# Optimization experiments

Hardware: AMD Instinct MI355X
Metric: run time of the kernel (lower is better)

The kernel has to match this reference:

```python
import jax, jax.numpy as jnp
import numpy as np

B, C, H, W = 8, 256, 128, 128
KC, VC, HEADS = 256, 256, 8


def setup_inputs() -> dict:
    key = jax.random.key(0)
    ks = jax.random.split(key, 10)
    s = 0.05
    return {
        "x": jax.random.normal(ks[0], (B, C, H, W), jnp.float32),
        "Wk": jax.random.normal(ks[1], (KC, C), jnp.float32) * s,
        "bk": jax.random.normal(ks[2], (KC,), jnp.float32) * s,
        "Wq": jax.random.normal(ks[3], (KC, C), jnp.float32) * s,
        "bq": jax.random.normal(ks[4], (KC,), jnp.float32) * s,
        "Wv": jax.random.normal(ks[5], (VC, C), jnp.float32) * s,
        "bv": jax.random.normal(ks[6], (VC,), jnp.float32) * s,
        "Wr": jax.random.normal(ks[7], (C, VC), jnp.float32) * s,
        "br": jax.random.normal(ks[8], (C,), jnp.float32) * s,
        "head_count": HEADS,
    }


def reference(x, Wk, bk, Wq, bq, Wv, bv, Wr, br, head_count):
    n, c, h, w = x.shape
    hw = h * w
    xf = x.reshape(n, c, hw)  # [n, C, S]
    # 1x1 convs == per-pixel linear projections
    keys = jnp.einsum('kc,ncs->nks', Wk, xf) + bk[None, :, None]
    queries = jnp.einsum('kc,ncs->nks', Wq, xf) + bq[None, :, None]
    values = jnp.einsum('vc,ncs->nvs', Wv, xf) + bv[None, :, None]

    dk = Wk.shape[0] // head_count
    dv = Wv.shape[0] // head_count
    # split heads along channel dim (matches torch channel slicing)
    K = jax.nn.softmax(keys.reshape(n, head_count, dk, hw), axis=-1)   # softmax over spatial
    Q = jax.nn.softmax(queries.reshape(n, head_count, dk, hw), axis=2) # softmax over key dim
    V = values.reshape(n, head_count, dv, hw)

    # context = K @ V^T : [n, h, dk, dv]
    ctx = jnp.einsum('nhks,nhvs->nhkv', K, V)
    # attended = ctx^T @ Q : [n, h, dv, S]
    att = jnp.einsum('nhkv,nhks->nhvs', ctx, Q).reshape(n, head_count * dv, h, w)

    attention = jnp.einsum('ov,nvhw->nohw', Wr, att) + br[None, :, None, None]
    # attention map: per-head mean over key dim, then mean over heads
    attention_map = K.mean(axis=2).mean(axis=1).reshape(n, h, w)
    # torch returns the LAST head's context (loop variable after the loop)
    context_last = ctx[:, -1]
    return attention, context_last, attention_map
```

## Files before the change

### kernel.cpp

```cpp
#include <hip/hip_runtime.h>
#include <hip/hip_bf16.h>

typedef float f32x4 __attribute__((ext_vector_type(4)));
typedef short s16x8 __attribute__((ext_vector_type(8)));
typedef short s16x4 __attribute__((ext_vector_type(4)));
typedef __bf16 bf16x8 __attribute__((ext_vector_type(8)));
typedef unsigned short u16;

#define DEVI __device__ __forceinline__

static constexpr int    HW      = 16384;
static constexpr size_t BSTRIDE = (size_t)256 * HW;

static constexpr size_t oXBT   = 0;
static constexpr size_t oEK    = oXBT  + (size_t)8 * HW * 256 * 2;
static constexpr size_t oQT    = oEK   + (size_t)8 * 256 * HW * 2;
static constexpr size_t oVB    = oQT   + (size_t)8 * HW * 256 * 2;
static constexpr size_t oWK    = oVB   + (size_t)8 * 256 * HW * 2;
static constexpr size_t oBIAS  = oWK   + (size_t)768 * 256 * 2;
static constexpr size_t oISE   = oBIAS + 4096;
static constexpr size_t oPS    = oISE  + 8192;
static constexpr size_t oCTX   = oPS   + (size_t)256 * 2048 * 4;
static constexpr size_t oMB    = oCTX  + (size_t)64 * 1024 * 4;
static constexpr size_t oCPART = oMB   + (size_t)8 * 256 * 256 * 2;
static constexpr size_t oMPART = oCPART + (size_t)4096 * 1024 * 4;

DEVI float bf2f(short x) {
  unsigned u = ((unsigned)(unsigned short)x) << 16;
  return __builtin_bit_cast(float, u);
}
DEVI u16 f2bf(float x) { return __builtin_bit_cast(u16, (__bf16)x); }

DEVI void gld16(const void* g, void* l) {
  __builtin_amdgcn_global_load_lds(
      (__attribute__((address_space(1))) void*)(g),
      (__attribute__((address_space(3))) void*)(l), 16, 0, 0);
}

__global__ __launch_bounds__(256) void k_prep(
    const float* __restrict__ Wk, const float* __restrict__ Wq, const float* __restrict__ Wv,
    const float* __restrict__ bk, const float* __restrict__ bq, const float* __restrict__ bv,
    u16* __restrict__ Wkqv, float* __restrict__ bias)
{
  int i = blockIdx.x * 256 + threadIdx.x;
  for (int p = i; p < 768 * 256; p += 64 * 256) {
    float v = (p < 65536) ? Wk[p] : (p < 131072 ? Wq[p - 65536] : Wv[p - 131072]);
    Wkqv[p] = f2bf(v);
  }
  if (i < 768) bias[i] = (i < 256) ? bk[i] : (i < 512 ? bq[i - 256] : bv[i - 512]);
}

__global__ __launch_bounds__(256) void k_transpose(const float* __restrict__ in_, u16* __restrict__ out)
{
  __shared__ u16 lds[64 * 256];
  const int t = threadIdx.x;
  const int n = blockIdx.y;
  const int s0 = blockIdx.x * 64;
  const float* src = in_ + ((size_t)n * 256 + t) * HW + s0;
  #pragma unroll
  for (int i = 0; i < 16; ++i) {
    f32x4 v = *(const f32x4*)(src + i * 4);
    #pragma unroll
    for (int j = 0; j < 4; ++j) lds[(i * 4 + j) * 256 + t] = f2bf(v[j]);
  }
  __syncthreads();
  s16x8* gp = (s16x8*)(out + (size_t)n * BSTRIDE + (size_t)s0 * 256);
  const s16x8* lp = (const s16x8*)lds;
  #pragma unroll
  for (int i = 0; i < 8; ++i) gp[t + i * 256] = lp[t + i * 256];
}


__global__ __launch_bounds__(256, 2) void k_projKV(
    const u16* __restrict__ W, const u16* __restrict__ xbT, const float* __restrict__ bias,
    u16* __restrict__ ek, u16* __restrict__ vb, float* __restrict__ ps)
{
  __shared__ u16 smem[32768];
  const int t = threadIdx.x;
  const int L = blockIdx.x;
  const int n = L & 7;
  const int idx = L >> 3;
  const int mbi = idx & 3;
  const int sq  = idx >> 2;
  const bool isK = (mbi < 2);
  const int m0 = (mbi & 1) * 128;
  const int aBase = (isK ? 0 : 512) + m0;
  const int lane = t & 63;
  const int l15 = lane & 15, l4 = (lane >> 4) & 3;
  const int wv = t >> 6;
  const int wm = (wv & 1) * 64, wn = (wv >> 1) * 64;
  const u16* Ab = W + (size_t)aBase * 256;
  const u16* Bb = xbT + (size_t)n * BSTRIDE;
  u16* Al = smem;
  u16* Bl = smem + 16384;

  float biasv[4];
  #pragma unroll
  for (int mf = 0; mf < 4; ++mf) biasv[mf] = bias[aBase + wm + mf * 16 + l15];

  const int rr = t >> 3;
  const int csh = t & 7;
  auto STAGE = [&](int buf, int it) {
    const int k0 = (it & 3) * 64;
    const size_t s_t0 = (size_t)((sq * 4 + (it >> 2)) * 128);
    #pragma unroll
    for (int i = 0; i < 4; ++i) {
      const int row = i * 32 + rr;
      const int cs = (csh ^ (row & 7)) * 8;
      gld16(Ab + (size_t)row * 256 + k0 + cs,          Al + buf * 8192 + i * 2048 + t * 8);
      gld16(Bb + (s_t0 + row) * 256 + k0 + cs,         Bl + buf * 8192 + i * 2048 + t * 8);
    }
  };

  f32x4 acc[4][4] = {};
  STAGE(0, 0); STAGE(1, 1);

  u16* outb = (isK ? ek : vb) + (size_t)n * BSTRIDE;

  #pragma unroll
  for (int it = 0; it < 16; ++it) {
    if (it == 15)                          asm volatile("s_waitcnt vmcnt(0)" ::: "memory");
    else if ((it & 3) <= 1 && it >= 4) {
      if (isK) asm volatile("s_waitcnt vmcnt(28)" ::: "memory");
      else     asm volatile("s_waitcnt vmcnt(24)" ::: "memory");
    } else                                 asm volatile("s_waitcnt vmcnt(8)" ::: "memory");
    __builtin_amdgcn_s_barrier();

    const int buf = it & 1;
    #pragma unroll
    for (int ks = 0; ks < 2; ++ks) {
      bf16x8 af[4], bff[4];
      #pragma unroll
      for (int g = 0; g < 4; ++g) {
        const int mrow = wm + g * 16 + l15;
        const int srow = wn + g * 16 + l15;
        af[g]  = *(const bf16x8*)&Al[buf * 8192 + mrow * 64 + (((ks * 4 + l4) ^ (mrow & 7)) * 8)];
        bff[g] = *(const bf16x8*)&Bl[buf * 8192 + srow * 64 + (((ks * 4 + l4) ^ (srow & 7)) * 8)];
      }
      __builtin_amdgcn_s_setprio(1);
      #pragma unroll
      for (int sf = 0; sf < 4; ++sf)
        #pragma unroll
        for (int mf = 0; mf < 4; ++mf)
          acc[sf][mf] = __builtin_amdgcn_mfma_f32_16x16x32_bf16(bff[sf], af[mf], acc[sf][mf], 0, 0, 0);
      __builtin_amdgcn_s_setprio(0);
    }
    asm volatile("s_waitcnt lgkmcnt(0)" ::: "memory");
    __builtin_amdgcn_s_barrier();
    if (it < 14) STAGE(buf, it + 2);

    if ((it & 3) == 3) {
      const int tile = it >> 2;
      const int s0t = (sq * 4 + tile) * 128;
      const int stile = sq * 4 + tile;
      if (isK) {
        float rs[4] = {0.f, 0.f, 0.f, 0.f};
        #pragma unroll
        for (int sf = 0; sf < 4; ++sf)
          #pragma unroll
          for (int mf = 0; mf < 4; ++mf) {
            s16x4 pk;
            #pragma unroll
            for (int r = 0; r < 4; ++r) {
              const float e = __expf(acc[sf][mf][r] + biasv[mf]);
              rs[mf] += e;
              pk[r] = (short)f2bf(e);
            }
            *(s16x4*)(outb + (size_t)(m0 + wm + mf * 16 + l15) * HW + s0t + wn + sf * 16 + l4 * 4) = pk;
          }
        #pragma unroll
        for (int mf = 0; mf < 4; ++mf) {
          float v = rs[mf];
          v += __shfl_xor(v, 16); v += __shfl_xor(v, 32);
          if (l4 == 0)
            ps[((size_t)(stile * 2 + (wn >> 6))) * 2048 + n * 256 + m0 + wm + mf * 16 + l15] = v;
        }
      } else {
        #pragma unroll
        for (int sf = 0; sf < 4; ++sf)
          #pragma unroll
          for (int mf = 0; mf < 4; ++mf) {
            s16x4 pk;
            #pragma unroll
            for (int r = 0; r < 4; ++r) pk[r] = (short)f2bf(acc[sf][mf][r] + biasv[mf]);
            *(s16x4*)(outb + (size_t)(m0 + wm + mf * 16 + l15) * HW + s0t + wn + sf * 16 + l4 * 4) = pk;
          }
      }
      #pragma unroll
      for (int sf = 0; sf < 4; ++sf)
        #pragma unroll
        for (int mf = 0; mf < 4; ++mf) acc[sf][mf] = f32x4{0.f, 0.f, 0.f, 0.f};
    }
  }
}

__global__ __launch_bounds__(256, 2) void k_attn2(
    const u16* __restrict__ Mb, const u16* __restrict__ qT, const float* __restrict__ br,
    float* __restrict__ Out)
{
  __shared__ u16 smem[32768];
  const int t = threadIdx.x;
  const int L = blockIdx.x;
  const int n = L & 7;
  const int idx = L >> 3;
  const int mb = idx & 1;
  const int sq = idx >> 1;
  const int m0 = mb * 128;
  const int lane = t & 63;
  const int l15 = lane & 15, l4 = (lane >> 4) & 3;
  const int wv = t >> 6;
  const int wm = (wv & 1) * 64, wn = (wv >> 1) * 64;
  const u16* Ab = Mb + (size_t)n * 65536 + (size_t)m0 * 256;
  const u16* Bb = qT + (size_t)n * BSTRIDE;
  u16* Al = smem;
  u16* Bl = smem + 16384;

  float biasv[4];
  #pragma unroll
  for (int mf = 0; mf < 4; ++mf) biasv[mf] = br[m0 + wm + mf * 16 + l15];

  const int rr = t >> 3;
  const int csh = t & 7;
  auto STAGE = [&](int buf, int it) {
    const int k0 = (it & 3) * 64;
    const size_t s_t0 = (size_t)((sq * 4 + (it >> 2)) * 128);
    #pragma unroll
    for (int i = 0; i < 4; ++i) {
      const int row = i * 32 + rr;
      const int cs = (csh ^ (row & 7)) * 8;
      gld16(Ab + (size_t)row * 256 + k0 + cs,  Al + buf * 8192 + i * 2048 + t * 8);
      gld16(Bb + (s_t0 + row) * 256 + k0 + cs, Bl + buf * 8192 + i * 2048 + t * 8);
    }
  };

  f32x4 acc[4][4] = {};
  STAGE(0, 0); STAGE(1, 1);

  float* ob = Out + (size_t)n * BSTRIDE;

  #pragma unroll
  for (int it = 0; it < 16; ++it) {
    if (it == 15)                          asm volatile("s_waitcnt vmcnt(0)" ::: "memory");
    else if ((it & 3) <= 1 && it >= 4)     asm volatile("s_waitcnt vmcnt(24)" ::: "memory");
    else                                   asm volatile("s_waitcnt vmcnt(8)" ::: "memory");
    __builtin_amdgcn_s_barrier();

    const int buf = it & 1;
    #pragma unroll
    for (int ks = 0; ks < 2; ++ks) {
      bf16x8 af[4], bff[4];
      #pragma unroll
      for (int g = 0; g < 4; ++g) {
        const int mrow = wm + g * 16 + l15;
        const int srow = wn + g * 16 + l15;
        af[g]  = *(const bf16x8*)&Al[buf * 8192 + mrow * 64 + (((ks * 4 + l4) ^ (mrow & 7)) * 8)];
        bff[g] = *(const bf16x8*)&Bl[buf * 8192 + srow * 64 + (((ks * 4 + l4) ^ (srow & 7)) * 8)];
      }
      __builtin_amdgcn_s_setprio(1);
      #pragma unroll
      for (int sf = 0; sf < 4; ++sf)
        #pragma unroll
        for (int mf = 0; mf < 4; ++mf)
          acc[sf][mf] = __builtin_amdgcn_mfma_f32_16x16x32_bf16(bff[sf], af[mf], acc[sf][mf], 0, 0, 0);
      __builtin_amdgcn_s_setprio(0);
    }
    asm volatile("s_waitcnt lgkmcnt(0)" ::: "memory");
    __builtin_amdgcn_s_barrier();
    if (it < 14) STAGE(buf, it + 2);

    if ((it & 3) == 3) {
      const int s0t = (sq * 4 + (it >> 2)) * 128;
      #pragma unroll
      for (int sf = 0; sf < 4; ++sf)
        #pragma unroll
        for (int mf = 0; mf < 4; ++mf) {
          f32x4 o = acc[sf][mf] + biasv[mf];
          *(f32x4*)(ob + (size_t)(m0 + wm + mf * 16 + l15) * HW + s0t + wn + sf * 16 + l4 * 4) = o;
          acc[sf][mf] = f32x4{0.f, 0.f, 0.f, 0.f};
        }
    }
  }
}

#define GEMM_CORE(Ab, Bb)                                                                   \
  u16* Al = smem;                                                                           \
  u16* Bl = smem + 16384;                                                                   \
  auto STAGE = [&](int buf, int kt) {                                                       \
    const int k0 = kt * 64;                                                                 \
    _Pragma("unroll")                                                                       \
    for (int i = 0; i < 4; ++i) {                                                           \
      const int r_ = i * 32 + (t >> 3);                                                     \
      const int cs = (((t & 7) ^ (r_ & 7)) * 8);                                            \
      gld16((Ab) + (size_t)r_ * 256 + k0 + cs, Al + buf * 8192 + i * 2048 + t * 8);         \
      gld16((Bb) + (size_t)r_ * 256 + k0 + cs, Bl + buf * 8192 + i * 2048 + t * 8);         \
    }                                                                                       \
  };                                                                                        \
  f32x4 acc[4][4] = {};                                                                     \
  STAGE(0, 0); STAGE(1, 1);                                                                 \
  _Pragma("unroll")                                                                         \
  for (int kt = 0; kt < 4; ++kt) {                                                          \
    if (kt < 3) asm volatile("s_waitcnt vmcnt(8)" ::: "memory");                            \
    else        asm volatile("s_waitcnt vmcnt(0)" ::: "memory");                            \
    __builtin_amdgcn_s_barrier();                                                           \
    const int buf = kt & 1;                                                                 \
    _Pragma("unroll")                                                                       \
    for (int ks = 0; ks < 2; ++ks) {                                                        \
      bf16x8 af[4], bff[4];                                                                 \
      _Pragma("unroll")                                                                     \
      for (int g = 0; g < 4; ++g) {                                                         \
        const int mrow = wm + g * 16 + l15;                                                 \
        const int srow = wn + g * 16 + l15;                                                 \
        af[g]  = *(const bf16x8*)&Al[buf * 8192 + mrow * 64 + (((ks * 4 + l4) ^ (mrow & 7)) * 8)]; \
        bff[g] = *(const bf16x8*)&Bl[buf * 8192 + srow * 64 + (((ks * 4 + l4) ^ (srow & 7)) * 8)]; \
      }                                                                                     \
      __builtin_amdgcn_s_setprio(1);                                                        \
      _Pragma("unroll")                                                                     \
      for (int mg = 0; mg < 4; ++mg)                                                        \
        _Pragma("unroll")                                                                   \
        for (int ng = 0; ng < 4; ++ng)                                                      \
          acc[mg][ng] = __builtin_amdgcn_mfma_f32_16x16x32_bf16(af[mg], bff[ng], acc[mg][ng], 0, 0, 0); \
      __builtin_amdgcn_s_setprio(0);                                                        \
    }                                                                                       \
    asm volatile("s_waitcnt lgkmcnt(0)" ::: "memory");                                      \
    __builtin_amdgcn_s_barrier();                                                           \
    if (kt < 2) STAGE(buf, kt + 2);                                                         \
  }

__global__ __launch_bounds__(256, 2) void k_projQ(
    const u16* __restrict__ W, const u16* __restrict__ xbT, const float* __restrict__ bias,
    u16* __restrict__ qT)
{
  __shared__ u16 smem[32768];
  const int t = threadIdx.x;
  const int L = blockIdx.x;
  const int n  = L & 7;
  const int idx = L >> 3;
  const int mbq = idx & 1;
  const int sb  = idx >> 1;
  const int m0 = 256 + mbq * 128, s0 = sb * 128;
  const int lane = t & 63;
  const int l15 = lane & 15, l4 = (lane >> 4) & 3;
  const int wv = t >> 6;
  const int wm = (wv & 1) * 64, wn = (wv >> 1) * 64;
  const u16* Ab = W + (size_t)m0 * 256;
  const u16* Bb = xbT + (size_t)n * BSTRIDE + (size_t)s0 * 256;

  GEMM_CORE(Ab, Bb)

  #pragma unroll
  for (int mg = 0; mg < 4; ++mg)
    #pragma unroll
    for (int r = 0; r < 4; ++r) {
      const float bb = bias[m0 + wm + mg * 16 + l4 * 4 + r];
      #pragma unroll
      for (int ng = 0; ng < 4; ++ng) acc[mg][ng][r] += bb;
    }

  #pragma unroll
  for (int hh = 0; hh < 2; ++hh)
    #pragma unroll
    for (int ng = 0; ng < 4; ++ng) {
      float s = 0.f;
      #pragma unroll
      for (int mg = hh * 2; mg < hh * 2 + 2; ++mg)
        #pragma unroll
        for (int r = 0; r < 4; ++r) { const float e = __expf(acc[mg][ng][r]); acc[mg][ng][r] = e; s += e; }
      s += __shfl_xor(s, 16);
      s += __shfl_xor(s, 32);
      const float inv = 1.f / s;
      #pragma unroll
      for (int mg = hh * 2; mg < hh * 2 + 2; ++mg)
        #pragma unroll
        for (int r = 0; r < 4; ++r) acc[mg][ng][r] *= inv;
    }
  __syncthreads();
  #pragma unroll
  for (int mg = 0; mg < 4; ++mg)
    #pragma unroll
    for (int ng = 0; ng < 4; ++ng)
      #pragma unroll
      for (int r = 0; r < 4; ++r) {
        const int srow = wn + ng * 16 + l15;
        const int mcol = wm + mg * 16 + l4 * 4 + r;
        smem[srow * 136 + mcol] = f2bf(acc[mg][ng][r]);
      }
  __syncthreads();
  u16* O = qT + (size_t)n * BSTRIDE + (size_t)s0 * 256 + mbq * 128;
  #pragma unroll
  for (int it = 0; it < 8; ++it) {
    const int row = it * 16 + (t >> 4);
    *(s16x8*)(O + (size_t)row * 256 + (t & 15) * 8) = *(const s16x8*)&smem[row * 136 + (t & 15) * 8];
  }
}

__global__ __launch_bounds__(256) void k_inv(const float* __restrict__ ps, float* __restrict__ ise)
{
  const int i = blockIdx.x * 256 + threadIdx.x;
  float s = 0.f;
  for (int b = 0; b < 256; ++b) s += ps[(size_t)b * 2048 + i];
  ise[i] = 1.f / s;
}

__global__ __launch_bounds__(64) void k_ctx_part(
    const u16* __restrict__ ek, const u16* __restrict__ vb, const float* __restrict__ ise,
    float* __restrict__ cpart, float* __restrict__ mpart)
{
  const int blk = blockIdx.x;
  const int chunk = blk & 63, nh = blk >> 6;
  const int h = nh & 7, n = nh >> 3;
  const int lane = threadIdx.x;
  const int l15 = lane & 15, l4 = lane >> 4;
  const u16* kb = ek + ((size_t)n * 256 + h * 32) * HW;
  const u16* vv = vb + ((size_t)n * 256 + h * 32) * HW;
  const float iv0 = ise[n * 256 + h * 32 + l15];
  const float iv1 = ise[n * 256 + h * 32 + 16 + l15];
  f32x4 acc[2][2] = {};
  float macc[8][8] = {};
  const int sbase = chunk * 256 + l4 * 8;
  #pragma unroll
  for (int ks = 0; ks < 8; ++ks) {
    const int sb = sbase + ks * 32;
    bf16x8 ef[2], vf[2];
    #pragma unroll
    for (int g = 0; g < 2; ++g) {
      ef[g] = *(const bf16x8*)(kb + (size_t)(g * 16 + l15) * HW + sb);
      vf[g] = *(const bf16x8*)(vv + (size_t)(g * 16 + l15) * HW + sb);
    }
    #pragma unroll
    for (int j = 0; j < 8; ++j)
      macc[ks][j] = fmaf(iv0, (float)ef[0][j], fmaf(iv1, (float)ef[1][j], macc[ks][j]));
    #pragma unroll
    for (int a = 0; a < 2; ++a)
      #pragma unroll
      for (int b = 0; b < 2; ++b)
        acc[a][b] = __builtin_amdgcn_mfma_f32_16x16x32_bf16(ef[a], vf[b], acc[a][b], 0, 0, 0);
  }
  float* op = cpart + (size_t)blk * 1024;
  #pragma unroll
  for (int a = 0; a < 2; ++a)
    #pragma unroll
    for (int b = 0; b < 2; ++b)
      #pragma unroll
      for (int r = 0; r < 4; ++r)
        op[(a * 16 + l4 * 4 + r) * 32 + b * 16 + l15] = acc[a][b][r];
  #pragma unroll
  for (int ks = 0; ks < 8; ++ks)
    #pragma unroll
    for (int j = 0; j < 8; ++j) {
      float v = macc[ks][j];
      v += __shfl_xor(v, 1); v += __shfl_xor(v, 2);
      v += __shfl_xor(v, 4); v += __shfl_xor(v, 8);
      macc[ks][j] = v;
    }
  if (l15 == 0) {
    float* mp = mpart + ((size_t)h * 8 + n) * HW + sbase;
    #pragma unroll
    for (int ks = 0; ks < 8; ++ks) {
      f32x4 a = {macc[ks][0], macc[ks][1], macc[ks][2], macc[ks][3]};
      f32x4 b = {macc[ks][4], macc[ks][5], macc[ks][6], macc[ks][7]};
      *(f32x4*)(mp + ks * 32)     = a;
      *(f32x4*)(mp + ks * 32 + 4) = b;
    }
  }
}

__global__ __launch_bounds__(256) void k_ctx_reduce(
    const float* __restrict__ cpart, const float* __restrict__ ise,
    float* __restrict__ ctx, float* __restrict__ dctx)
{
  const int nh = blockIdx.x, n = nh >> 3, h = nh & 7, t = threadIdx.x;
  f32x4 a = {};
  for (int c = 0; c < 64; ++c) a += *(const f32x4*)(cpart + ((size_t)nh * 64 + c) * 1024 + t * 4);
  const float inv = ise[n * 256 + h * 32 + (t >> 3)];
  a *= inv;
  *(f32x4*)(ctx + (size_t)nh * 1024 + t * 4) = a;
  if (h == 7) *(f32x4*)(dctx + (size_t)n * 1024 + t * 4) = a;
}

__global__ __launch_bounds__(256) void k_mmat(
    const float* __restrict__ ctx, const float* __restrict__ Wr, u16* __restrict__ Mb)
{
  const int nh = blockIdx.x, n = nh >> 3, h = nh & 7, o = threadIdx.x;
  __shared__ float cl[1024];
  #pragma unroll
  for (int i = 0; i < 4; ++i) cl[o + i * 256] = ctx[(size_t)nh * 1024 + o + i * 256];
  __syncthreads();
  float wr[32];
  const float* wp = Wr + (size_t)o * 256 + h * 32;
  #pragma unroll
  for (int v = 0; v < 32; ++v) wr[v] = wp[v];
  u16* mp = Mb + ((size_t)n * 256 + o) * 256 + h * 32;
  #pragma unroll 4
  for (int k = 0; k < 32; ++k) {
    float s = 0.f;
    #pragma unroll
    for (int v = 0; v < 32; ++v) s += wr[v] * cl[k * 32 + v];
    mp[k] = f2bf(s);
  }
}

__global__ __launch_bounds__(256) void k_map_reduce(const float* __restrict__ mpart, float* __restrict__ dmap)
{
  const int i = blockIdx.x * 256 + threadIdx.x;
  f32x4 a = {};
  #pragma unroll
  for (int h = 0; h < 8; ++h) a += *(const f32x4*)(mpart + (size_t)h * 131072 + (size_t)i * 4);
  a *= (1.0f / 256.0f);
  *(f32x4*)(dmap + (size_t)i * 4) = a;
}

extern "C" void kernel_launch(void* const* d_in, const int* in_sizes, int n_in,
                              void* d_out, int out_size, void* d_ws, size_t ws_size,
                              hipStream_t stream)
{
  (void)in_sizes; (void)n_in; (void)out_size; (void)ws_size;
  const float* x  = (const float*)d_in[0];
  const float* Wk = (const float*)d_in[1];
  const float* bk = (const float*)d_in[2];
  const float* Wq = (const float*)d_in[3];
  const float* bq = (const float*)d_in[4];
  const float* Wv = (const float*)d_in[5];
  const float* bv = (const float*)d_in[6];
  const float* Wr = (const float*)d_in[7];
  const float* br = (const float*)d_in[8];

  char* ws = (char*)d_ws;
  u16*   xbT  = (u16*)(ws + oXBT);
  u16*   ek   = (u16*)(ws + oEK);
  u16*   qT   = (u16*)(ws + oQT);
  u16*   vb   = (u16*)(ws + oVB);
  u16*   Wkqv = (u16*)(ws + oWK);
  float* bias = (float*)(ws + oBIAS);
  float* ise  = (float*)(ws + oISE);
  float* ps   = (float*)(ws + oPS);
  float* ctx  = (float*)(ws + oCTX);
  u16*   Mb   = (u16*)(ws + oMB);
  float* cpart= (float*)(ws + oCPART);
  float* mpart= (float*)(ws + oMPART);

  float* attn = (float*)d_out;
  float* dctx = (float*)d_out + 33554432;
  float* dmap = (float*)d_out + 33562624;

  k_prep<<<64, 256, 0, stream>>>(Wk, Wq, Wv, bk, bq, bv, Wkqv, bias);
  k_transpose<<<dim3(256, 8), 256, 0, stream>>>(x, xbT);
  k_projKV<<<1024, 256, 0, stream>>>(Wkqv, xbT, bias, ek, vb, ps);
  k_inv<<<8, 256, 0, stream>>>(ps, ise);
  k_projQ<<<2048, 256, 0, stream>>>(Wkqv, xbT, bias, qT);
  k_ctx_part<<<4096, 64, 0, stream>>>(ek, vb, ise, cpart, mpart);
  k_ctx_reduce<<<64, 256, 0, stream>>>(cpart, ise, ctx, dctx);
  k_mmat<<<64, 256, 0, stream>>>(ctx, Wr, Mb);
  k_map_reduce<<<128, 256, 0, stream>>>(mpart, dmap);
  k_attn2<<<512, 256, 0, stream>>>(Mb, qT, br, attn);
}
```

Baseline: 289.7 us.

## Merge K/V and Q projections into one 256x256-tile 8-wave GEMM kernel

```diff
diff --git a/kernel.cpp b/kernel.cpp
--- a/kernel.cpp
+++ b/kernel.cpp
@@ -70,126 +70,175 @@
   for (int i = 0; i < 8; ++i) gp[t + i * 256] = lp[t + i * 256];
 }
 
-
-__global__ __launch_bounds__(256, 2) void k_projKV(
+__global__ __launch_bounds__(512, 2) void k_proj8(
     const u16* __restrict__ W, const u16* __restrict__ xbT, const float* __restrict__ bias,
-    u16* __restrict__ ek, u16* __restrict__ vb, float* __restrict__ ps)
-{
-  __shared__ u16 smem[32768];
+    u16* __restrict__ ek, u16* __restrict__ qT, u16* __restrict__ vb, float* __restrict__ ps)
+{
+  __shared__ u16 smem[65536];
   const int t = threadIdx.x;
   const int L = blockIdx.x;
   const int n = L & 7;
   const int idx = L >> 3;
-  const int mbi = idx & 3;
-  const int sq  = idx >> 2;
-  const bool isK = (mbi < 2);
-  const int m0 = (mbi & 1) * 128;
-  const int aBase = (isK ? 0 : 512) + m0;
+  const int mb = idx % 3;
+  const int sb = idx / 3;
   const int lane = t & 63;
   const int l15 = lane & 15, l4 = (lane >> 4) & 3;
-  const int wv = t >> 6;
-  const int wm = (wv & 1) * 64, wn = (wv >> 1) * 64;
-  const u16* Ab = W + (size_t)aBase * 256;
-  const u16* Bb = xbT + (size_t)n * BSTRIDE;
-  u16* Al = smem;
-  u16* Bl = smem + 16384;
-
-  float biasv[4];
-  #pragma unroll
-  for (int mf = 0; mf < 4; ++mf) biasv[mf] = bias[aBase + wm + mf * 16 + l15];
-
-  const int rr = t >> 3;
-  const int csh = t & 7;
-  auto STAGE = [&](int buf, int it) {
-    const int k0 = (it & 3) * 64;
-    const size_t s_t0 = (size_t)((sq * 4 + (it >> 2)) * 128);
-    #pragma unroll
-    for (int i = 0; i < 4; ++i) {
-      const int row = i * 32 + rr;
-      const int cs = (csh ^ (row & 7)) * 8;
-      gld16(Ab + (size_t)row * 256 + k0 + cs,          Al + buf * 8192 + i * 2048 + t * 8);
-      gld16(Bb + (s_t0 + row) * 256 + k0 + cs,         Bl + buf * 8192 + i * 2048 + t * 8);
+  const int w = t >> 6;
+  const int wr = w & 1, wc = w >> 1;
+
+  const u16* Ag = W + (size_t)mb * 65536;
+  const u16* Bg = xbT + (size_t)n * BSTRIDE;
+
+  float biasv[8];
+  #pragma unroll
+  for (int mf = 0; mf < 8; ++mf) biasv[mf] = bias[mb * 256 + wr * 128 + mf * 16 + l15];
+
+  const int srow8 = t >> 3, schk = t & 7;
+
+  auto STAGE = [&](int kt, int u) {
+    const int buf = kt & 1;
+    const int h = u & 1;
+    const int k0 = (kt & 3) * 64;
+    #pragma unroll
+    for (int i = 0; i < 2; ++i) {
+      const int rl = h * 128 + i * 64 + srow8;
+      const int cs = (schk ^ (rl & 7)) * 8;
+      if (u < 2) {
+        gld16(Bg + ((size_t)((sb * 2 + (kt >> 2)) * 256 + rl)) * 256 + k0 + cs,
+              smem + 32768 + buf * 16384 + h * 8192 + i * 4096 + t * 8);
+      } else {
+        gld16(Ag + (size_t)rl * 256 + k0 + cs,
+              smem + buf * 16384 + h * 8192 + i * 4096 + t * 8);
+      }
     }
   };
 
-  f32x4 acc[4][4] = {};
-  STAGE(0, 0); STAGE(1, 1);
-
-  u16* outb = (isK ? ek : vb) + (size_t)n * BSTRIDE;
-
-  #pragma unroll
-  for (int it = 0; it < 16; ++it) {
-    if (it == 15)                          asm volatile("s_waitcnt vmcnt(0)" ::: "memory");
-    else if ((it & 3) <= 1 && it >= 4) {
-      if (isK) asm volatile("s_waitcnt vmcnt(28)" ::: "memory");
-      else     asm volatile("s_waitcnt vmcnt(24)" ::: "memory");
-    } else                                 asm volatile("s_waitcnt vmcnt(8)" ::: "memory");
-    __builtin_amdgcn_s_barrier();
-
-    const int buf = it & 1;
-    #pragma unroll
-    for (int ks = 0; ks < 2; ++ks) {
-      bf16x8 af[4], bff[4];
-      #pragma unroll
-      for (int g = 0; g < 4; ++g) {
-        const int mrow = wm + g * 16 + l15;
-        const int srow = wn + g * 16 + l15;
-        af[g]  = *(const bf16x8*)&Al[buf * 8192 + mrow * 64 + (((ks * 4 + l4) ^ (mrow & 7)) * 8)];
-        bff[g] = *(const bf16x8*)&Bl[buf * 8192 + srow * 64 + (((ks * 4 + l4) ^ (srow & 7)) * 8)];
-      }
+  f32x4 acc[8][4] = {};
+  bf16x8 bff[4][2];
+
+  STAGE(0, 0); STAGE(0, 1); STAGE(0, 2); STAGE(0, 3);
+
+  u16* ekb = ek + (size_t)n * BSTRIDE;
+  u16* vbb = vb + (size_t)n * BSTRIDE;
+  u16* qtb = qT + (size_t)n * BSTRIDE;
+
+  #pragma unroll
+  for (int kt = 0; kt < 8; ++kt) {
+    const int buf = kt & 1;
+    #pragma unroll
+    for (int q = 0; q < 4; ++q) {
+      if (q == 0) {
+        if (kt < 7) STAGE(kt + 1, 0);
+        if (kt == 0)      asm volatile("s_waitcnt vmcnt(2)" ::: "memory");
+        else if (kt == 7) asm volatile("s_waitcnt vmcnt(0)" ::: "memory");
+        else if (kt == 4) {
+          if (mb == 0)      asm volatile("s_waitcnt vmcnt(42)" ::: "memory");
+          else if (mb == 2) asm volatile("s_waitcnt vmcnt(34)" ::: "memory");
+          else              asm volatile("s_waitcnt vmcnt(63)" ::: "memory");
+        }
+        else              asm volatile("s_waitcnt vmcnt(2)" ::: "memory");
+        __builtin_amdgcn_s_barrier();
+        #pragma unroll
+        for (int sf = 0; sf < 4; ++sf) {
+          const int srow = wc * 64 + sf * 16 + l15;
+          #pragma unroll
+          for (int ks = 0; ks < 2; ++ks)
+            bff[sf][ks] = *(const bf16x8*)&smem[32768 + buf * 16384 + srow * 64 +
+                                                (((ks * 4 + l4) ^ (srow & 7)) * 8)];
+        }
+      }
+      bf16x8 af[2][2];
+      #pragma unroll
+      for (int j = 0; j < 2; ++j) {
+        const int mrow = wr * 128 + (q * 2 + j) * 16 + l15;
+        #pragma unroll
+        for (int ks = 0; ks < 2; ++ks)
+          af[j][ks] = *(const bf16x8*)&smem[buf * 16384 + mrow * 64 +
+                                            (((ks * 4 + l4) ^ (mrow & 7)) * 8)];
+      }
+      if (q > 0) {
+        if (kt < 7) STAGE(kt + 1, q);
+        __builtin_amdgcn_s_barrier();
+      }
+      asm volatile("s_waitcnt lgkmcnt(0)" ::: "memory");
+      __builtin_amdgcn_sched_barrier(0);
       __builtin_amdgcn_s_setprio(1);
       #pragma unroll
-      for (int sf = 0; sf < 4; ++sf)
-        #pragma unroll
-        for (int mf = 0; mf < 4; ++mf)
-          acc[sf][mf] = __builtin_amdgcn_mfma_f32_16x16x32_bf16(bff[sf], af[mf], acc[sf][mf], 0, 0, 0);
-      __builtin_amdgcn_s_setprio(0);
-    }
-    asm volatile("s_waitcnt lgkmcnt(0)" ::: "memory");
-    __builtin_amdgcn_s_barrier();
-    if (it < 14) STAGE(buf, it + 2);
-
-    if ((it & 3) == 3) {
-      const int tile = it >> 2;
-      const int s0t = (sq * 4 + tile) * 128;
-      const int stile = sq * 4 + tile;
-      if (isK) {
-        float rs[4] = {0.f, 0.f, 0.f, 0.f};
+      for (int j = 0; j < 2; ++j)
         #pragma unroll
         for (int sf = 0; sf < 4; ++sf)
           #pragma unroll
-          for (int mf = 0; mf < 4; ++mf) {
+          for (int ks = 0; ks < 2; ++ks)
+            acc[q * 2 + j][sf] = __builtin_amdgcn_mfma_f32_16x16x32_bf16(
+                bff[sf][ks], af[j][ks], acc[q * 2 + j][sf], 0, 0, 0);
+      __builtin_amdgcn_s_setprio(0);
+      __builtin_amdgcn_s_barrier();
+    }
+
+    if ((kt & 3) == 3) {
+      const int st = kt >> 2;
+      const int s0t = (sb * 2 + st) * 256 + wc * 64;
+      const int slot = (sb * 2 + st) * 4 + wc;
+      if (mb == 0) {
+        float rs[8];
+        #pragma unroll
+        for (int mf = 0; mf < 8; ++mf) rs[mf] = 0.f;
+        #pragma unroll
+        for (int mf = 0; mf < 8; ++mf) {
+          const size_t rb = (size_t)(wr * 128 + mf * 16 + l15) * HW + s0t;
+          #pragma unroll
+          for (int sf = 0; sf < 4; ++sf) {
             s16x4 pk;
             #pragma unroll
             for (int r = 0; r < 4; ++r) {
-              const float e = __expf(acc[sf][mf][r] + biasv[mf]);
+              const float e = __expf(acc[mf][sf][r] + biasv[mf]);
               rs[mf] += e;
               pk[r] = (short)f2bf(e);
             }
-            *(s16x4*)(outb + (size_t)(m0 + wm + mf * 16 + l15) * HW + s0t + wn + sf * 16 + l4 * 4) = pk;
+            *(s16x4*)(ekb + rb + sf * 16 + l4 * 4) = pk;
           }
-        #pragma unroll
-        for (int mf = 0; mf < 4; ++mf) {
+        }
+        #pragma unroll
+        for (int mf = 0; mf < 8; ++mf) {
           float v = rs[mf];
           v += __shfl_xor(v, 16); v += __shfl_xor(v, 32);
-          if (l4 == 0)
-            ps[((size_t)(stile * 2 + (wn >> 6))) * 2048 + n * 256 + m0 + wm + mf * 16 + l15] = v;
-        }
-      } else {
-        #pragma unroll
-        for (int sf = 0; sf < 4; ++sf)
+          if (l4 == 0) ps[(size_t)slot * 2048 + n * 256 + wr * 128 + mf * 16 + l15] = v;
+        }
+      } else if (mb == 2) {
+        #pragma unroll
+        for (int mf = 0; mf < 8; ++mf) {
+          const size_t rb = (size_t)(wr * 128 + mf * 16 + l15) * HW + s0t;
           #pragma unroll
-          for (int mf = 0; mf < 4; ++mf) {
+          for (int sf = 0; sf < 4; ++sf) {
             s16x4 pk;
             #pragma unroll
-            for (int r = 0; r < 4; ++r) pk[r] = (short)f2bf(acc[sf][mf][r] + biasv[mf]);
-            *(s16x4*)(outb + (size_t)(m0 + wm + mf * 16 + l15) * HW + s0t + wn + sf * 16 + l4 * 4) = pk;
+            for (int r = 0; r < 4; ++r) pk[r] = (short)f2bf(acc[mf][sf][r] + biasv[mf]);
+            *(s16x4*)(vbb + rb + sf * 16 + l4 * 4) = pk;
           }
-      }
-      #pragma unroll
-      for (int sf = 0; sf < 4; ++sf)
-        #pragma unroll
-        for (int mf = 0; mf < 4; ++mf) acc[sf][mf] = f32x4{0.f, 0.f, 0.f, 0.f};
+        }
+      } else {
+        #pragma unroll
+        for (int hh = 0; hh < 4; ++hh) {
+          #pragma unroll
+          for (int sf = 0; sf < 4; ++sf)
+            #pragma unroll
+            for (int r = 0; r < 4; ++r) {
+              const float e0 = __expf(acc[2 * hh][sf][r]     + biasv[2 * hh]);
+              const float e1 = __expf(acc[2 * hh + 1][sf][r] + biasv[2 * hh + 1]);
+              float s_ = e0 + e1;
+              s_ += __shfl_xor(s_, 1); s_ += __shfl_xor(s_, 2);
+              s_ += __shfl_xor(s_, 4); s_ += __shfl_xor(s_, 8);
+              const float inv = 1.f / s_;
+              u16* qp = qtb + (size_t)(s0t + sf * 16 + l4 * 4 + r) * 256 + wr * 128 + hh * 32 + l15;
+              qp[0]  = f2bf(e0 * inv);
+              qp[16] = f2bf(e1 * inv);
+            }
+        }
+      }
+      #pragma unroll
+      for (int mf = 0; mf < 8; ++mf)
+        #pragma unroll
+        for (int sf = 0; sf < 4; ++sf) acc[mf][sf] = f32x4{0.f, 0.f, 0.f, 0.f};
     }
   }
 }
@@ -282,117 +331,6 @@
   }
 }
 
-#define GEMM_CORE(Ab, Bb)                                                                   \
-  u16* Al = smem;                                                                           \
-  u16* Bl = smem + 16384;                                                                   \
-  auto STAGE = [&](int buf, int kt) {                                                       \
-    const int k0 = kt * 64;                                                                 \
-    _Pragma("unroll")                                                                       \
-    for (int i = 0; i < 4; ++i) {                                                           \
-      const int r_ = i * 32 + (t >> 3);                                                     \
-      const int cs = (((t & 7) ^ (r_ & 7)) * 8);                                            \
-      gld16((Ab) + (size_t)r_ * 256 + k0 + cs, Al + buf * 8192 + i * 2048 + t * 8);         \
-      gld16((Bb) + (size_t)r_ * 256 + k0 + cs, Bl + buf * 8192 + i * 2048 + t * 8);         \
-    }                                                                                       \
-  };                                                                                        \
-  f32x4 acc[4][4] = {};                                                                     \
-  STAGE(0, 0); STAGE(1, 1);                                                                 \
-  _Pragma("unroll")                                                                         \
-  for (int kt = 0; kt < 4; ++kt) {                                                          \
-    if (kt < 3) asm volatile("s_waitcnt vmcnt(8)" ::: "memory");                            \
-    else        asm volatile("s_waitcnt vmcnt(0)" ::: "memory");                            \
-    __builtin_amdgcn_s_barrier();                                                           \
-    const int buf = kt & 1;                                                                 \
-    _Pragma("unroll")                                                                       \
-    for (int ks = 0; ks < 2; ++ks) {                                                        \
-      bf16x8 af[4], bff[4];                                                                 \
-      _Pragma("unroll")                                                                     \
-      for (int g = 0; g < 4; ++g) {                                                         \
-        const int mrow = wm + g * 16 + l15;                                                 \
-        const int srow = wn + g * 16 + l15;                                                 \
-        af[g]  = *(const bf16x8*)&Al[buf * 8192 + mrow * 64 + (((ks * 4 + l4) ^ (mrow & 7)) * 8)]; \
-        bff[g] = *(const bf16x8*)&Bl[buf * 8192 + srow * 64 + (((ks * 4 + l4) ^ (srow & 7)) * 8)]; \
-      }                                                                                     \
-      __builtin_amdgcn_s_setprio(1);                                                        \
-      _Pragma("unroll")                                                                     \
-      for (int mg = 0; mg < 4; ++mg)                                                        \
-        _Pragma("unroll")                                                                   \
-        for (int ng = 0; ng < 4; ++ng)                                                      \
-          acc[mg][ng] = __builtin_amdgcn_mfma_f32_16x16x32_bf16(af[mg], bff[ng], acc[mg][ng], 0, 0, 0); \
-      __builtin_amdgcn_s_setprio(0);                                                        \
-    }                                                                                       \
-    asm volatile("s_waitcnt lgkmcnt(0)" ::: "memory");                                      \
-    __builtin_amdgcn_s_barrier();                                                           \
-    if (kt < 2) STAGE(buf, kt + 2);                                                         \
-  }
-
-__global__ __launch_bounds__(256, 2) void k_projQ(
-    const u16* __restrict__ W, const u16* __restrict__ xbT, const float* __restrict__ bias,
-    u16* __restrict__ qT)
-{
-  __shared__ u16 smem[32768];
-  const int t = threadIdx.x;
-  const int L = blockIdx.x;
-  const int n  = L & 7;
-  const int idx = L >> 3;
-  const int mbq = idx & 1;
-  const int sb  = idx >> 1;
-  const int m0 = 256 + mbq * 128, s0 = sb * 128;
-  const int lane = t & 63;
-  const int l15 = lane & 15, l4 = (lane >> 4) & 3;
-  const int wv = t >> 6;
-  const int wm = (wv & 1) * 64, wn = (wv >> 1) * 64;
-  const u16* Ab = W + (size_t)m0 * 256;
-  const u16* Bb = xbT + (size_t)n * BSTRIDE + (size_t)s0 * 256;
-
-  GEMM_CORE(Ab, Bb)
-
-  #pragma unroll
-  for (int mg = 0; mg < 4; ++mg)
-    #pragma unroll
-    for (int r = 0; r < 4; ++r) {
-      const float bb = bias[m0 + wm + mg * 16 + l4 * 4 + r];
-      #pragma unroll
-      for (int ng = 0; ng < 4; ++ng) acc[mg][ng][r] += bb;
-    }
-
-  #pragma unroll
-  for (int hh = 0; hh < 2; ++hh)
-    #pragma unroll
-    for (int ng = 0; ng < 4; ++ng) {
-      float s = 0.f;
-      #pragma unroll
-      for (int mg = hh * 2; mg < hh * 2 + 2; ++mg)
-        #pragma unroll
-        for (int r = 0; r < 4; ++r) { const float e = __expf(acc[mg][ng][r]); acc[mg][ng][r] = e; s += e; }
-      s += __shfl_xor(s, 16);
-      s += __shfl_xor(s, 32);
-      const float inv = 1.f / s;
-      #pragma unroll
-      for (int mg = hh * 2; mg < hh * 2 + 2; ++mg)
-        #pragma unroll
-        for (int r = 0; r < 4; ++r) acc[mg][ng][r] *= inv;
-    }
-  __syncthreads();
-  #pragma unroll
-  for (int mg = 0; mg < 4; ++mg)
-    #pragma unroll
-    for (int ng = 0; ng < 4; ++ng)
-      #pragma unroll
-      for (int r = 0; r < 4; ++r) {
-        const int srow = wn + ng * 16 + l15;
-        const int mcol = wm + mg * 16 + l4 * 4 + r;
-        smem[srow * 136 + mcol] = f2bf(acc[mg][ng][r]);
-      }
-  __syncthreads();
-  u16* O = qT + (size_t)n * BSTRIDE + (size_t)s0 * 256 + mbq * 128;
-  #pragma unroll
-  for (int it = 0; it < 8; ++it) {
-    const int row = it * 16 + (t >> 4);
-    *(s16x8*)(O + (size_t)row * 256 + (t & 15) * 8) = *(const s16x8*)&smem[row * 136 + (t & 15) * 8];
-  }
-}
-
 __global__ __launch_bounds__(256) void k_inv(const float* __restrict__ ps, float* __restrict__ ise)
 {
   const int i = blockIdx.x * 256 + threadIdx.x;
@@ -544,9 +482,8 @@
 
   k_prep<<<64, 256, 0, stream>>>(Wk, Wq, Wv, bk, bq, bv, Wkqv, bias);
   k_transpose<<<dim3(256, 8), 256, 0, stream>>>(x, xbT);
-  k_projKV<<<1024, 256, 0, stream>>>(Wkqv, xbT, bias, ek, vb, ps);
+  k_proj8<<<768, 512, 0, stream>>>(Wkqv, xbT, bias, ek, qT, vb, ps);
   k_inv<<<8, 256, 0, stream>>>(ps, ise);
-  k_projQ<<<2048, 256, 0, stream>>>(Wkqv, xbT, bias, qT);
   k_ctx_part<<<4096, 64, 0, stream>>>(ek, vb, ise, cpart, mpart);
   k_ctx_reduce<<<64, 256, 0, stream>>>(cpart, ise, ctx, dctx);
   k_mmat<<<64, 256, 0, stream>>>(ctx, Wr, Mb);
```

New measurement: 299.9 us. 3.5% more time.
